# Kernel optimization log

Measured on AMD Instinct MI355X. Metric: run time of the kernel, lower is better.

Reference implementation:

```python
import jax, jax.numpy as jnp
import numpy as np

DIM, PASTLEN, BATCH, NSTEPS, HID = 128, 1, 4096, 50, 100
DELTA, P_ENT = 0.5, 0.0001
TRIL = DIM * (DIM + 1) // 2  # 8256
IN_DIM = DIM * PASTLEN


def _dense_init(key, fan_in, fan_out):
    kw, kb = jax.random.split(key)
    s = np.sqrt(2.0 / (fan_in + fan_out)).astype(np.float32)
    return (jax.random.normal(kw, (fan_in, fan_out), jnp.float32) * s,
            jnp.zeros((fan_out,), jnp.float32))


def setup_inputs() -> dict:
    key = jax.random.key(0)
    ks = jax.random.split(key, 3)
    inp = {
        'init_state': jax.random.normal(ks[0], (PASTLEN, BATCH, DIM), jnp.float32),
        'yhat': jax.random.normal(ks[1], (NSTEPS, BATCH, DIM), jnp.float32),
        'z': jax.random.normal(ks[2], (NSTEPS, BATCH, DIM, 1), jnp.float32),
        'ntimesteps': NSTEPS,
        'start': 0,
    }
    for pi, pre in enumerate(('drift', 'diff')):
        out_dim = DIM if pre == 'drift' else TRIL
        shapes = [(IN_DIM, HID, '1'), (HID, HID, '2'), (HID, HID, '3'), (HID, out_dim, 'o')]
        for li, (fi, fo, tag) in enumerate(shapes):
            W, b = _dense_init(jax.random.fold_in(key, 10 + pi * 4 + li), fi, fo)
            inp[f'{pre}_W{tag}'] = W
            inp[f'{pre}_b{tag}'] = b
    return inp


def _mlp(x, W1, b1, W2, b2, W3, b3, Wo, bo):
    # dense1(tanh) -> dense2(tanh) -> dense3(skip from h1, then relu) -> output
    h1 = jnp.tanh(x @ W1 + b1)
    h2 = jnp.tanh(h1 @ W2 + b2)
    h3 = jax.nn.relu((h2 + h1) @ W3 + b3)
    return h3 @ Wo + bo


def _fill_triangular(v):
    # tfp.math.fill_triangular (lower): concat(v[n:], reverse(v)) -> reshape (n,n) -> tril
    cat = jnp.concatenate([v[:, DIM:], v[:, ::-1]], axis=-1)
    return jnp.tril(cat.reshape(v.shape[0], DIM, DIM))


def _forward(init_state, yhat, z, drift_params, diff_params):
    sw = 1.0 / NSTEPS
    idx = jnp.arange(DIM)

    def scan_fn(carry, inputs):
        z_i, yhat_i = inputs  # (B, DIM, 1), (B, DIM)
        x = jnp.transpose(carry, (1, 0, 2)).reshape(BATCH, IN_DIM)
        last = carry[-1][:, :DIM]
        drift = _mlp(x, *drift_params)                    # (B, DIM)
        L = _fill_triangular(_mlp(x, *diff_params))       # (B, DIM, DIM)
        diag = jnp.exp(L[:, idx, idx])                    # exp on diagonal
        L = L.at[:, idx, idx].set(diag)
        det = jnp.prod(diag, axis=1)                      # (B,)
        out = last + drift + jnp.squeeze(L @ z_i, -1)     # Euler-Maruyama step
        # keras Huber (mean reduction) with scalar sample_weight, minus entropy term
        err = out - yhat_i
        ae = jnp.abs(err)
        hub = jnp.where(ae <= DELTA, 0.5 * err * err, DELTA * ae - 0.5 * DELTA * DELTA)
        loss_i = jnp.mean(hub) * sw - jnp.mean(jnp.log(det)) * sw * P_ENT
        new_carry = jnp.concatenate([carry[1:], out[None]], axis=0)
        return new_carry, loss_i

    _, losses = jax.lax.scan(scan_fn, init_state, (z, yhat))
    return jnp.cumsum(losses[::-1])[::-1]  # reverse cumsum, as in solve()


def reference(init_state, yhat, z, ntimesteps, start,
              drift_W1, drift_b1, drift_W2, drift_b2, drift_W3, drift_b3, drift_Wo, drift_bo,
              diff_W1, diff_b1, diff_W2, diff_b2, diff_W3, diff_b3, diff_Wo, diff_bo):
    drift_params = (drift_W1, drift_b1, drift_W2, drift_b2, drift_W3, drift_b3, drift_Wo, drift_bo)
    diff_params = (diff_W1, diff_b1, diff_W2, diff_b2, diff_W3, diff_b3, diff_Wo, diff_bo)
    return _forward(init_state, yhat, z, drift_params, diff_params)
```

## Files before the change

kernel.cpp:

```cpp
#include <hip/hip_runtime.h>
#include <math.h>

#define BATCHN 4096
#define DIMN 128
#define HIDN 100
#define NSTEPSN 50
#define KPAD 8192
#define HPN 101
#define HP4 104
#define KSLICES 4

struct Weights {
  const float *W1d,*b1d,*W2d,*b2d,*W3d,*b3d,*Wod,*bod;
  const float *W1f,*b1f,*W2f,*b2f,*W3f,*b3f;
  const float *Wdiag,*bdiag;
};

__device__ inline int tri_row(int k) {
  float rf = (1.0f + sqrtf(1.0f + 8.0f*(float)k)) * 0.5f;
  int r = (int)rf;
  if (k < (r*(r-1))/2) --r;
  else if (k >= (r*(r+1))/2) ++r;
  return r;
}
__device__ inline int cat_vidx(int r, int c) {
  int kk = r*128 + c;
  return (kk < 8128) ? (kk + 128) : (16383 - kk);
}

__global__ __launch_bounds__(256) void init_wperm(const float* __restrict__ Wo,
    const float* __restrict__ bo, float* __restrict__ Wperm)
{
  int idx = blockIdx.x*256 + threadIdx.x;
  if (idx >= HP4*KPAD) return;
  int h = idx >> 13, k = idx & (KPAD-1);
  float val = 0.f;
  if (k < 8128 && h <= HIDN) {
    int r = tri_row(k);
    int c = k - (r*(r-1))/2;
    int vidx = cat_vidx(r, c);
    val = (h < HIDN) ? Wo[h*8256 + vidx] : bo[vidx];
  }
  Wperm[idx] = val;
}

__global__ __launch_bounds__(256) void init_misc(const float* __restrict__ Wo,
    const float* __restrict__ bo, float* __restrict__ Wdiag,
    float* __restrict__ bdiag)
{
  int idx = blockIdx.x*256 + threadIdx.x;
  if (idx < HIDN*128) {
    int h = idx >> 7, r = idx & 127;
    Wdiag[idx] = Wo[h*8256 + cat_vidx(r, r)];
  } else if (idx < HIDN*128 + 128) {
    int r = idx - HIDN*128;
    bdiag[r] = bo[cat_vidx(r, r)];
  }
}

__global__ __launch_bounds__(256) void init_pack(Weights wt, float* __restrict__ Wpack)
{
  int idx = blockIdx.x*256 + threadIdx.x;
  if (idx >= 6*128*128) return;
  int m = idx >> 14, rem = idx & 16383, c = rem >> 7, j = rem & 127;
  const float* src; int K;
  switch (m) {
    case 0: src = wt.W1d; K = 128; break;
    case 1: src = wt.W2d; K = 100; break;
    case 2: src = wt.W3d; K = 100; break;
    case 3: src = wt.W1f; K = 128; break;
    case 4: src = wt.W2f; K = 100; break;
    default: src = wt.W3f; K = 100; break;
  }
  Wpack[idx] = (j < HIDN && c < K) ? src[c*HIDN + j] : 0.f;
}

__global__ __launch_bounds__(256) void mlp_kernel(
    const float* __restrict__ xin, const float* __restrict__ E4prev,
    const float* __restrict__ yhat_prev,
    const float* __restrict__ z_t, Weights wt, const float* __restrict__ Wpack,
    float* __restrict__ xbase_out, float* __restrict__ h3b,
    float* __restrict__ hub_sum, float* __restrict__ ent_sum, int t)
{
  __shared__ float Wl[128*128];
  __shared__ float xinl[16*132];
  __shared__ float hA[16*132];
  __shared__ float hB[16*132];
  __shared__ float redw[4];
  __shared__ float redh[16];

  const int tid = threadIdx.x;
  const int b0 = blockIdx.x * 16;
  const int bb = tid >> 4;
  const int jt = tid & 15;
  const int j0 = jt * 8;

  {
    const int f = tid * 8;
    const int lb = f >> 7, c = f & 127;
    const float* xp = xin + (size_t)(b0+lb)*DIMN + c;
    float4 x0 = *(const float4*)xp;
    float4 x1 = *(const float4*)(xp+4);
    if (E4prev) {
      #pragma unroll
      for (int s = 0; s < KSLICES; ++s) {
        const float* ep = E4prev + ((size_t)s*BATCHN + b0+lb)*DIMN + c;
        const float4 e0 = *(const float4*)ep;
        const float4 e1 = *(const float4*)(ep+4);
        x0.x+=e0.x; x0.y+=e0.y; x0.z+=e0.z; x0.w+=e0.w;
        x1.x+=e1.x; x1.y+=e1.y; x1.z+=e1.z; x1.w+=e1.w;
      }
    }
    *(float4*)&xinl[lb*132+c]   = x0;
    *(float4*)&xinl[lb*132+c+4] = x1;
    if (yhat_prev) {
      const float* yp = yhat_prev + (size_t)(b0+lb)*DIMN + c;
      float4 y0 = *(const float4*)yp;
      float4 y1 = *(const float4*)(yp+4);
      float xv[8] = {x0.x,x0.y,x0.z,x0.w,x1.x,x1.y,x1.z,x1.w};
      float yv[8] = {y0.x,y0.y,y0.z,y0.w,y1.x,y1.y,y1.z,y1.w};
      float hub = 0.f;
      #pragma unroll
      for (int i=0;i<8;++i) {
        float e = xv[i]-yv[i], ae = fabsf(e);
        hub += (ae <= 0.5f) ? 0.5f*e*e : fmaf(0.5f, ae, -0.125f);
      }
      #pragma unroll
      for (int off=32; off>0; off>>=1) hub += __shfl_down(hub, off);
      if ((tid & 63) == 0) redw[tid>>6] = hub;
    }
  }
  __syncthreads();
  if (yhat_prev && tid == 0)
    atomicAdd(&hub_sum[t-1], redw[0]+redw[1]+redw[2]+redw[3]);

  float acc[8];

  auto stage = [&](const float* __restrict__ Wg, int K) {
    __syncthreads();
    for (int i = tid*4; i < K*128; i += 1024)
      *(float4*)&Wl[i] = *(const float4*)&Wg[i];
    __syncthreads();
  };
  auto compute = [&](const float* inl, int K) {
    #pragma unroll
    for (int i=0;i<8;++i) acc[i] = 0.f;
    const float* inrow = inl + bb*132;
    #pragma unroll 4
    for (int c = 0; c < K; ++c) {
      const float xv = inrow[c];
      const float4 w0 = *(const float4*)&Wl[c*128 + j0];
      const float4 w1 = *(const float4*)&Wl[c*128 + j0 + 4];
      acc[0] = fmaf(xv, w0.x, acc[0]);
      acc[1] = fmaf(xv, w0.y, acc[1]);
      acc[2] = fmaf(xv, w0.z, acc[2]);
      acc[3] = fmaf(xv, w0.w, acc[3]);
      acc[4] = fmaf(xv, w1.x, acc[4]);
      acc[5] = fmaf(xv, w1.y, acc[5]);
      acc[6] = fmaf(xv, w1.z, acc[6]);
      acc[7] = fmaf(xv, w1.w, acc[7]);
    }
  };

  const float* P_W1d = Wpack;
  const float* P_W2d = Wpack + 16384;
  const float* P_W3d = Wpack + 32768;
  const float* P_W1f = Wpack + 49152;
  const float* P_W2f = Wpack + 65536;
  const float* P_W3f = Wpack + 81920;

  float h1reg[8], driftreg[8];

  stage(P_W1d, 128); compute(xinl, 128);
  #pragma unroll
  for (int i=0;i<8;++i) {
    int j = j0+i;
    float v = (j < HIDN) ? tanhf(acc[i] + wt.b1d[j]) : 0.f;
    h1reg[i] = v; hA[bb*132+j] = v;
  }
  stage(P_W2d, 100); compute(hA, 100);
  #pragma unroll
  for (int i=0;i<8;++i) {
    int j = j0+i;
    float v = (j < HIDN) ? (tanhf(acc[i] + wt.b2d[j]) + h1reg[i]) : 0.f;
    hB[bb*132+j] = v;
  }
  stage(P_W3d, 100); compute(hB, 100);
  #pragma unroll
  for (int i=0;i<8;++i) {
    int j = j0+i;
    float v = (j < HIDN) ? fmaxf(acc[i] + wt.b3d[j], 0.f) : 0.f;
    hA[bb*132+j] = v;
  }
  stage(wt.Wod, 100); compute(hA, 100);
  #pragma unroll
  for (int i=0;i<8;++i) driftreg[i] = acc[i] + wt.bod[j0+i];

  stage(P_W1f, 128); compute(xinl, 128);
  #pragma unroll
  for (int i=0;i<8;++i) {
    int j = j0+i;
    float v = (j < HIDN) ? tanhf(acc[i] + wt.b1f[j]) : 0.f;
    h1reg[i] = v; hB[bb*132+j] = v;
  }
  stage(P_W2f, 100); compute(hB, 100);
  #pragma unroll
  for (int i=0;i<8;++i) {
    int j = j0+i;
    float v = (j < HIDN) ? (tanhf(acc[i] + wt.b2f[j]) + h1reg[i]) : 0.f;
    hA[bb*132+j] = v;
  }
  stage(P_W3f, 100); compute(hA, 100);
  {
    float sv[8];
    #pragma unroll
    for (int i=0;i<8;++i) {
      int j = j0+i;
      float v = (j < HIDN) ? fmaxf(acc[i] + wt.b3f[j], 0.f) : 0.f;
      hB[bb*132+j] = v;
      sv[i] = (j < HIDN) ? v : ((j == HIDN) ? 1.f : 0.f);
    }
    if (j0 < HP4) {
      float* hp = h3b + (size_t)(b0+bb)*HP4 + j0;
      *(float4*)hp     = make_float4(sv[0],sv[1],sv[2],sv[3]);
      *(float4*)(hp+4) = make_float4(sv[4],sv[5],sv[6],sv[7]);
    }
  }
  stage(wt.Wdiag, 100); compute(hB, 100);

  {
    float entacc = 0.f;
    const float* zp = z_t + (size_t)(b0+bb)*DIMN + j0;
    const float* xrow = xinl + bb*132 + j0;
    float o8[8];
    #pragma unroll
    for (int i=0;i<8;++i) {
      int j = j0+i;
      float vd = acc[i] + wt.bdiag[j];
      entacc += vd;
      o8[i] = xrow[i] + driftreg[i] + expf(vd) * zp[i];
    }
    float* bp = xbase_out + (size_t)(b0+bb)*DIMN + j0;
    *(float4*)bp     = make_float4(o8[0],o8[1],o8[2],o8[3]);
    *(float4*)(bp+4) = make_float4(o8[4],o8[5],o8[6],o8[7]);
    #pragma unroll
    for (int off=8; off>0; off>>=1) entacc += __shfl_down(entacc, off, 16);
    if (jt == 0) redh[bb] = entacc;
    __syncthreads();
    if (tid == 0) {
      float s = 0.f;
      #pragma unroll
      for (int i=0;i<16;++i) s += redh[i];
      atomicAdd(&ent_sum[t], s);
    }
  }
}

__global__ __launch_bounds__(256, 4) void heavy_kernel(
    const float* __restrict__ h3b,
    const float* __restrict__ Wperm,
    const float* __restrict__ z_t,
    float* __restrict__ E4)
{
  __shared__ float h3l[16*112];
  __shared__ float zl[16*128];
  __shared__ float El[16*128];

  const int tid = threadIdx.x;
  const int b0 = blockIdx.x * 16;
  const int slice = blockIdx.y;

  {
    const int b = tid >> 4, hs = tid & 15;
    float4* dst = (float4*)(h3l + b*112);
    const float4* src = (const float4*)(h3b + (size_t)(b0+b)*HP4);
    for (int c = hs; c < HP4/4; c += 16) dst[c] = src[c];
  }
  for (int i = tid; i < 16*128; i += 256) {
    int bbi = i >> 7, c = i & 127;
    zl[i] = z_t[(size_t)(b0+bbi)*DIMN + c];
    El[i] = 0.f;
  }
  __syncthreads();

  const int bq = tid >> 6;
  const int kq = tid & 63;
  const float* h3p = h3l + bq*4*112;

  for (int w = slice*4; w < slice*4 + 4; ++w) {
    const int k0 = w*512 + kq*8;
    float acc[4][8];
    #pragma unroll
    for (int bi=0;bi<4;++bi)
      #pragma unroll
      for (int i=0;i<8;++i) acc[bi][i] = 0.f;

    const float* wp = Wperm + k0;
    #pragma unroll 2
    for (int hc = 0; hc < HP4/4; ++hc) {
      float hcol[4][4];
      *(float4*)&hcol[0][0] = *(const float4*)&h3p[hc*4];
      *(float4*)&hcol[1][0] = *(const float4*)&h3p[112 + hc*4];
      *(float4*)&hcol[2][0] = *(const float4*)&h3p[224 + hc*4];
      *(float4*)&hcol[3][0] = *(const float4*)&h3p[336 + hc*4];
      #pragma unroll
      for (int hh = 0; hh < 4; ++hh) {
        const size_t hrow = (size_t)(hc*4+hh)*KPAD;
        const float4 wa = *(const float4*)&wp[hrow];
        const float4 wb = *(const float4*)&wp[hrow + 4];
        const float w8[8] = {wa.x,wa.y,wa.z,wa.w, wb.x,wb.y,wb.z,wb.w};
        #pragma unroll
        for (int bi=0; bi<4; ++bi) {
          const float hv = hcol[bi][hh];
          #pragma unroll
          for (int i=0;i<8;++i) acc[bi][i] = fmaf(hv, w8[i], acc[bi][i]);
        }
      }
    }

    if (k0 < 8128) {
      int kr[8], kc[8];
      #pragma unroll
      for (int i=0;i<8;++i) {
        int k = k0 + i;
        int r = tri_row(k);
        kr[i] = r;
        kc[i] = k - (r*(r-1))/2;
      }
      #pragma unroll
      for (int bi=0;bi<4;++bi) {
        const int b = bq*4 + bi;
        float run = 0.f; int cur = kr[0];
        #pragma unroll
        for (int i=0;i<8;++i) {
          float p = acc[bi][i] * zl[b*128 + kc[i]];
          if (kr[i] == cur) run += p;
          else { atomicAdd(&El[b*128 + cur], run); cur = kr[i]; run = p; }
        }
        atomicAdd(&El[b*128 + cur], run);
      }
    }
  }
  __syncthreads();

  {
    float* eout = E4 + ((size_t)slice*BATCHN + b0)*DIMN;
    const int i = tid*8;
    *(float4*)&eout[i]   = *(const float4*)&El[i];
    *(float4*)&eout[i+4] = *(const float4*)&El[i+4];
  }
}

__global__ __launch_bounds__(256) void huber_kernel(const float* __restrict__ xb,
    const float* __restrict__ E4, const float* __restrict__ y,
    float* __restrict__ dst)
{
  __shared__ float r[4];
  int idx = blockIdx.x*256 + threadIdx.x;
  float hub = 0.f;
  for (int i4 = idx; i4 < BATCHN*DIMN/4; i4 += 256*256) {
    float4 x = ((const float4*)xb)[i4];
    #pragma unroll
    for (int s=0;s<KSLICES;++s) {
      const float4 e = ((const float4*)E4)[(size_t)s*(BATCHN*DIMN/4) + i4];
      x.x+=e.x; x.y+=e.y; x.z+=e.z; x.w+=e.w;
    }
    const float4 yv = ((const float4*)y)[i4];
    float ev[4] = {x.x-yv.x, x.y-yv.y, x.z-yv.z, x.w-yv.w};
    #pragma unroll
    for (int i=0;i<4;++i) {
      float ae = fabsf(ev[i]);
      hub += (ae <= 0.5f) ? 0.5f*ev[i]*ev[i] : fmaf(0.5f, ae, -0.125f);
    }
  }
  #pragma unroll
  for (int off=32; off>0; off>>=1) hub += __shfl_down(hub, off);
  if ((threadIdx.x & 63) == 0) r[threadIdx.x>>6] = hub;
  __syncthreads();
  if (threadIdx.x == 0) atomicAdd(dst, r[0]+r[1]+r[2]+r[3]);
}

__global__ void finalize_kernel(const float* __restrict__ hub_sum,
    const float* __restrict__ ent_sum, float* __restrict__ out)
{
  int i = threadIdx.x;
  if (i < NSTEPSN) {
    const float c1 = (1.0f/NSTEPSN)/(float)(BATCHN*DIMN);
    const float c2 = (1.0f/NSTEPSN)*0.0001f/(float)BATCHN;
    float s = 0.f;
    for (int j = NSTEPSN-1; j >= i; --j) s += hub_sum[j]*c1 - ent_sum[j]*c2;
    out[i] = s;
  }
}

extern "C" void kernel_launch(void* const* d_in, const int* in_sizes, int n_in,
                              void* d_out, int out_size, void* d_ws, size_t ws_size,
                              hipStream_t stream) {
  const float* init_state = (const float*)d_in[0];
  const float* yhat = (const float*)d_in[1];
  const float* z    = (const float*)d_in[2];
  Weights wt;
  wt.W1d = (const float*)d_in[5];  wt.b1d = (const float*)d_in[6];
  wt.W2d = (const float*)d_in[7];  wt.b2d = (const float*)d_in[8];
  wt.W3d = (const float*)d_in[9];  wt.b3d = (const float*)d_in[10];
  wt.Wod = (const float*)d_in[11]; wt.bod = (const float*)d_in[12];
  wt.W1f = (const float*)d_in[13]; wt.b1f = (const float*)d_in[14];
  wt.W2f = (const float*)d_in[15]; wt.b2f = (const float*)d_in[16];
  wt.W3f = (const float*)d_in[17]; wt.b3f = (const float*)d_in[18];
  const float* diff_Wo = (const float*)d_in[19];
  const float* diff_bo = (const float*)d_in[20];

  float* ws = (float*)d_ws;
  float* Wperm  = ws;
  float* Wdiag  = Wperm + (size_t)HP4*KPAD;
  float* bdiag  = Wdiag + HIDN*128;
  float* h3b    = bdiag + 128;
  float* xbA    = h3b + (size_t)BATCHN*HP4;
  float* xbB    = xbA + (size_t)BATCHN*DIMN;
  float* E4     = xbB + (size_t)BATCHN*DIMN;
  float* Wpack  = E4 + (size_t)KSLICES*BATCHN*DIMN;
  float* hub_sum = Wpack + 6*128*128;
  float* ent_sum = hub_sum + 64;

  wt.Wdiag = Wdiag; wt.bdiag = bdiag;

  hipMemsetAsync(hub_sum, 0, 128*sizeof(float), stream);
  init_wperm<<<(HP4*KPAD)/256, 256, 0, stream>>>(diff_Wo, diff_bo, Wperm);
  init_misc<<<(HIDN*128 + 128 + 255)/256, 256, 0, stream>>>(
      diff_Wo, diff_bo, Wdiag, bdiag);
  init_pack<<<(6*128*128)/256, 256, 0, stream>>>(wt, Wpack);

  const float* xin = init_state;
  const float* e4in = nullptr;
  for (int t = 0; t < NSTEPSN; ++t) {
    float* xbout = (t & 1) ? xbB : xbA;
    const float* zt = z + (size_t)t*BATCHN*DIMN;
    const float* yp = t ? (yhat + (size_t)(t-1)*BATCHN*DIMN) : nullptr;
    mlp_kernel<<<256, 256, 0, stream>>>(xin, e4in, yp, zt, wt, Wpack,
                                        xbout, h3b, hub_sum, ent_sum, t);
    heavy_kernel<<<dim3(256, KSLICES), 256, 0, stream>>>(h3b, Wperm, zt, E4);
    xin = xbout; e4in = E4;
  }
  huber_kernel<<<256, 256, 0, stream>>>(xin, E4,
      yhat + (size_t)(NSTEPSN-1)*BATCHN*DIMN, hub_sum + (NSTEPSN-1));
  finalize_kernel<<<1, 64, 0, stream>>>(hub_sum, ent_sum, (float*)d_out);
}
```

Before: 10.92 ms.

## Split heavy kernel into more K-slices and drop shared-memory weight staging

The heavy kernel's K dimension is split into 8 slices instead of 4, doubling the grid and raising the occupancy hint, so each block processes fewer 512-wide chunks. The h3 shared-memory staging in the heavy kernel is removed, and each thread now reads h3 rows straight from global memory. The MLP kernel no longer copies each weight matrix into a 64KB LDS buffer between syncs and reads weights directly from global/L2 with float4 input loads. This removes syncs and LDS pressure but adds redundant global traffic and doubles the partial-sum buffer that the next step must reduce.

```diff
diff --git a/kernel.cpp b/kernel.cpp
--- a/kernel.cpp
+++ b/kernel.cpp
@@ -8,7 +8,8 @@
 #define KPAD 8192
 #define HPN 101
 #define HP4 104
-#define KSLICES 4
+#define KSLICES 8
+#define WPS (16/KSLICES)
 
 struct Weights {
   const float *W1d,*b1d,*W2d,*b2d,*W3d,*b3d,*Wod,*bod;
@@ -76,13 +77,12 @@
 }
 
 __global__ __launch_bounds__(256) void mlp_kernel(
-    const float* __restrict__ xin, const float* __restrict__ E4prev,
+    const float* __restrict__ xin, const float* __restrict__ Eprev,
     const float* __restrict__ yhat_prev,
     const float* __restrict__ z_t, Weights wt, const float* __restrict__ Wpack,
     float* __restrict__ xbase_out, float* __restrict__ h3b,
     float* __restrict__ hub_sum, float* __restrict__ ent_sum, int t)
 {
-  __shared__ float Wl[128*128];
   __shared__ float xinl[16*132];
   __shared__ float hA[16*132];
   __shared__ float hB[16*132];
@@ -101,10 +101,10 @@
     const float* xp = xin + (size_t)(b0+lb)*DIMN + c;
     float4 x0 = *(const float4*)xp;
     float4 x1 = *(const float4*)(xp+4);
-    if (E4prev) {
+    if (Eprev) {
       #pragma unroll
       for (int s = 0; s < KSLICES; ++s) {
-        const float* ep = E4prev + ((size_t)s*BATCHN + b0+lb)*DIMN + c;
+        const float* ep = Eprev + ((size_t)s*BATCHN + b0+lb)*DIMN + c;
         const float4 e0 = *(const float4*)ep;
         const float4 e1 = *(const float4*)(ep+4);
         x0.x+=e0.x; x0.y+=e0.y; x0.z+=e0.z; x0.w+=e0.w;
@@ -136,29 +136,29 @@
 
   float acc[8];
 
-  auto stage = [&](const float* __restrict__ Wg, int K) {
-    __syncthreads();
-    for (int i = tid*4; i < K*128; i += 1024)
-      *(float4*)&Wl[i] = *(const float4*)&Wg[i];
-    __syncthreads();
-  };
-  auto compute = [&](const float* inl, int K) {
+  auto compute = [&](const float* inl, const float* __restrict__ Wg, int K) {
     #pragma unroll
     for (int i=0;i<8;++i) acc[i] = 0.f;
     const float* inrow = inl + bb*132;
-    #pragma unroll 4
-    for (int c = 0; c < K; ++c) {
-      const float xv = inrow[c];
-      const float4 w0 = *(const float4*)&Wl[c*128 + j0];
-      const float4 w1 = *(const float4*)&Wl[c*128 + j0 + 4];
-      acc[0] = fmaf(xv, w0.x, acc[0]);
-      acc[1] = fmaf(xv, w0.y, acc[1]);
-      acc[2] = fmaf(xv, w0.z, acc[2]);
-      acc[3] = fmaf(xv, w0.w, acc[3]);
-      acc[4] = fmaf(xv, w1.x, acc[4]);
-      acc[5] = fmaf(xv, w1.y, acc[5]);
-      acc[6] = fmaf(xv, w1.z, acc[6]);
-      acc[7] = fmaf(xv, w1.w, acc[7]);
+    const float* wrow = Wg + j0;
+    #pragma unroll 2
+    for (int c4 = 0; c4 < K; c4 += 4) {
+      const float4 xq = *(const float4*)&inrow[c4];
+      const float xs[4] = {xq.x, xq.y, xq.z, xq.w};
+      #pragma unroll
+      for (int cc = 0; cc < 4; ++cc) {
+        const float4 w0 = *(const float4*)&wrow[(size_t)(c4+cc)*128];
+        const float4 w1 = *(const float4*)&wrow[(size_t)(c4+cc)*128 + 4];
+        const float xv = xs[cc];
+        acc[0] = fmaf(xv, w0.x, acc[0]);
+        acc[1] = fmaf(xv, w0.y, acc[1]);
+        acc[2] = fmaf(xv, w0.z, acc[2]);
+        acc[3] = fmaf(xv, w0.w, acc[3]);
+        acc[4] = fmaf(xv, w1.x, acc[4]);
+        acc[5] = fmaf(xv, w1.y, acc[5]);
+        acc[6] = fmaf(xv, w1.z, acc[6]);
+        acc[7] = fmaf(xv, w1.w, acc[7]);
+      }
     }
   };
 
@@ -171,46 +171,46 @@
 
   float h1reg[8], driftreg[8];
 
-  stage(P_W1d, 128); compute(xinl, 128);
+  compute(xinl, P_W1d, 128);
   #pragma unroll
   for (int i=0;i<8;++i) {
     int j = j0+i;
     float v = (j < HIDN) ? tanhf(acc[i] + wt.b1d[j]) : 0.f;
     h1reg[i] = v; hA[bb*132+j] = v;
   }
-  stage(P_W2d, 100); compute(hA, 100);
+  compute(hA, P_W2d, 100);
   #pragma unroll
   for (int i=0;i<8;++i) {
     int j = j0+i;
     float v = (j < HIDN) ? (tanhf(acc[i] + wt.b2d[j]) + h1reg[i]) : 0.f;
     hB[bb*132+j] = v;
   }
-  stage(P_W3d, 100); compute(hB, 100);
+  compute(hB, P_W3d, 100);
   #pragma unroll
   for (int i=0;i<8;++i) {
     int j = j0+i;
     float v = (j < HIDN) ? fmaxf(acc[i] + wt.b3d[j], 0.f) : 0.f;
     hA[bb*132+j] = v;
   }
-  stage(wt.Wod, 100); compute(hA, 100);
+  compute(hA, wt.Wod, 100);
   #pragma unroll
   for (int i=0;i<8;++i) driftreg[i] = acc[i] + wt.bod[j0+i];
 
-  stage(P_W1f, 128); compute(xinl, 128);
+  compute(xinl, P_W1f, 128);
   #pragma unroll
   for (int i=0;i<8;++i) {
     int j = j0+i;
     float v = (j < HIDN) ? tanhf(acc[i] + wt.b1f[j]) : 0.f;
     h1reg[i] = v; hB[bb*132+j] = v;
   }
-  stage(P_W2f, 100); compute(hB, 100);
+  compute(hB, P_W2f, 100);
   #pragma unroll
   for (int i=0;i<8;++i) {
     int j = j0+i;
     float v = (j < HIDN) ? (tanhf(acc[i] + wt.b2f[j]) + h1reg[i]) : 0.f;
     hA[bb*132+j] = v;
   }
-  stage(P_W3f, 100); compute(hA, 100);
+  compute(hA, P_W3f, 100);
   {
     float sv[8];
     #pragma unroll
@@ -226,7 +226,7 @@
       *(float4*)(hp+4) = make_float4(sv[4],sv[5],sv[6],sv[7]);
     }
   }
-  stage(wt.Wdiag, 100); compute(hB, 100);
+  compute(hB, wt.Wdiag, 100);
 
   {
     float entacc = 0.f;
@@ -256,13 +256,12 @@
   }
 }
 
-__global__ __launch_bounds__(256, 4) void heavy_kernel(
+__global__ __launch_bounds__(256, 8) void heavy_kernel(
     const float* __restrict__ h3b,
     const float* __restrict__ Wperm,
     const float* __restrict__ z_t,
-    float* __restrict__ E4)
-{
-  __shared__ float h3l[16*112];
+    float* __restrict__ Eout)
+{
   __shared__ float zl[16*128];
   __shared__ float El[16*128];
 
@@ -270,12 +269,6 @@
   const int b0 = blockIdx.x * 16;
   const int slice = blockIdx.y;
 
-  {
-    const int b = tid >> 4, hs = tid & 15;
-    float4* dst = (float4*)(h3l + b*112);
-    const float4* src = (const float4*)(h3b + (size_t)(b0+b)*HP4);
-    for (int c = hs; c < HP4/4; c += 16) dst[c] = src[c];
-  }
   for (int i = tid; i < 16*128; i += 256) {
     int bbi = i >> 7, c = i & 127;
     zl[i] = z_t[(size_t)(b0+bbi)*DIMN + c];
@@ -285,9 +278,12 @@
 
   const int bq = tid >> 6;
   const int kq = tid & 63;
-  const float* h3p = h3l + bq*4*112;
-
-  for (int w = slice*4; w < slice*4 + 4; ++w) {
+  const float* h3p0 = h3b + (size_t)(b0 + bq*4 + 0)*HP4;
+  const float* h3p1 = h3b + (size_t)(b0 + bq*4 + 1)*HP4;
+  const float* h3p2 = h3b + (size_t)(b0 + bq*4 + 2)*HP4;
+  const float* h3p3 = h3b + (size_t)(b0 + bq*4 + 3)*HP4;
+
+  for (int w = slice*WPS; w < slice*WPS + WPS; ++w) {
     const int k0 = w*512 + kq*8;
     float acc[4][8];
     #pragma unroll
@@ -299,10 +295,10 @@
     #pragma unroll 2
     for (int hc = 0; hc < HP4/4; ++hc) {
       float hcol[4][4];
-      *(float4*)&hcol[0][0] = *(const float4*)&h3p[hc*4];
-      *(float4*)&hcol[1][0] = *(const float4*)&h3p[112 + hc*4];
-      *(float4*)&hcol[2][0] = *(const float4*)&h3p[224 + hc*4];
-      *(float4*)&hcol[3][0] = *(const float4*)&h3p[336 + hc*4];
+      *(float4*)&hcol[0][0] = *(const float4*)&h3p0[hc*4];
+      *(float4*)&hcol[1][0] = *(const float4*)&h3p1[hc*4];
+      *(float4*)&hcol[2][0] = *(const float4*)&h3p2[hc*4];
+      *(float4*)&hcol[3][0] = *(const float4*)&h3p3[hc*4];
       #pragma unroll
       for (int hh = 0; hh < 4; ++hh) {
         const size_t hrow = (size_t)(hc*4+hh)*KPAD;
@@ -344,7 +340,7 @@
   __syncthreads();
 
   {
-    float* eout = E4 + ((size_t)slice*BATCHN + b0)*DIMN;
+    float* eout = Eout + ((size_t)slice*BATCHN + b0)*DIMN;
     const int i = tid*8;
     *(float4*)&eout[i]   = *(const float4*)&El[i];
     *(float4*)&eout[i+4] = *(const float4*)&El[i+4];
@@ -352,7 +348,7 @@
 }
 
 __global__ __launch_bounds__(256) void huber_kernel(const float* __restrict__ xb,
-    const float* __restrict__ E4, const float* __restrict__ y,
+    const float* __restrict__ E, const float* __restrict__ y,
     float* __restrict__ dst)
 {
   __shared__ float r[4];
@@ -362,7 +358,7 @@
     float4 x = ((const float4*)xb)[i4];
     #pragma unroll
     for (int s=0;s<KSLICES;++s) {
-      const float4 e = ((const float4*)E4)[(size_t)s*(BATCHN*DIMN/4) + i4];
+      const float4 e = ((const float4*)E)[(size_t)s*(BATCHN*DIMN/4) + i4];
       x.x+=e.x; x.y+=e.y; x.z+=e.z; x.w+=e.w;
     }
     const float4 yv = ((const float4*)y)[i4];
@@ -417,8 +413,8 @@
   float* h3b    = bdiag + 128;
   float* xbA    = h3b + (size_t)BATCHN*HP4;
   float* xbB    = xbA + (size_t)BATCHN*DIMN;
-  float* E4     = xbB + (size_t)BATCHN*DIMN;
-  float* Wpack  = E4 + (size_t)KSLICES*BATCHN*DIMN;
+  float* Ebuf   = xbB + (size_t)BATCHN*DIMN;
+  float* Wpack  = Ebuf + (size_t)KSLICES*BATCHN*DIMN;
   float* hub_sum = Wpack + 6*128*128;
   float* ent_sum = hub_sum + 64;
 
@@ -431,17 +427,17 @@
   init_pack<<<(6*128*128)/256, 256, 0, stream>>>(wt, Wpack);
 
   const float* xin = init_state;
-  const float* e4in = nullptr;
+  const float* ein = nullptr;
   for (int t = 0; t < NSTEPSN; ++t) {
     float* xbout = (t & 1) ? xbB : xbA;
     const float* zt = z + (size_t)t*BATCHN*DIMN;
     const float* yp = t ? (yhat + (size_t)(t-1)*BATCHN*DIMN) : nullptr;
-    mlp_kernel<<<256, 256, 0, stream>>>(xin, e4in, yp, zt, wt, Wpack,
+    mlp_kernel<<<256, 256, 0, stream>>>(xin, ein, yp, zt, wt, Wpack,
                                         xbout, h3b, hub_sum, ent_sum, t);
-    heavy_kernel<<<dim3(256, KSLICES), 256, 0, stream>>>(h3b, Wperm, zt, E4);
-    xin = xbout; e4in = E4;
-  }
-  huber_kernel<<<256, 256, 0, stream>>>(xin, E4,
+    heavy_kernel<<<dim3(256, KSLICES), 256, 0, stream>>>(h3b, Wperm, zt, Ebuf);
+    xin = xbout; ein = Ebuf;
+  }
+  huber_kernel<<<256, 256, 0, stream>>>(xin, Ebuf,
       yhat + (size_t)(NSTEPSN-1)*BATCHN*DIMN, hub_sum + (NSTEPSN-1));
   finalize_kernel<<<1, 64, 0, stream>>>(hub_sum, ent_sum, (float*)d_out);
 }
```

After: 15.33 ms. 1.4x slower.
